# Kernel tuning notes

Measured on AMD Instinct MI355X. Metric: run time of the kernel, lower is better.

The kernel has to match this reference:

```python
import jax, jax.numpy as jnp
import numpy as np
from jax import lax

# 4th-order Butterworth lowpass, scipy.signal.butter(4, 0.2)
B_COEF = np.array([0.004824343357716228, 0.019297373430864913, 0.02894606014629737,
                   0.019297373430864913, 0.004824343357716228], dtype=np.float32)
A_COEF = np.array([1.0, -2.369513007182038, 2.3139884144006453,
                   -1.0546654058785672, 0.18737949236818502], dtype=np.float32)


def setup_inputs() -> dict:
    key = jax.random.key(0)
    x = jax.random.normal(key, (8, 64, 48000), dtype=jnp.float32)
    return {"x": x, "b": jnp.asarray(B_COEF), "a": jnp.asarray(A_COEF)}


def _pad_odd(x, n):
    # Faithful to torch _pad_odd (including its exact slicing on the right side).
    left = 2.0 * x[..., 0:1] - jnp.flip(x[..., 0:n], axis=-1)
    right = 2.0 * x[..., -1:] - jnp.flip(x[..., -(n + 2):-2], axis=-1)
    return jnp.concatenate([left, x, right], axis=-1)


def _lfilter(x, a, b):
    # y[n] = (sum_k b[k] x[n-k] - sum_j a[j] y[n-j]) / a[0]
    a0 = a[0]
    bn = b / a0
    an = a[1:] / a0                      # [N], N = order
    ntaps = b.shape[0]                   # static
    N = a.shape[0] - 1                   # static
    T = x.shape[-1]
    # FIR part: small static tap loop, fully vectorized over batch/time.
    pad = [(0, 0)] * (x.ndim - 1) + [(ntaps - 1, 0)]
    xp = jnp.pad(x, pad)
    f = bn[0] * xp[..., ntaps - 1: ntaps - 1 + T]
    for k in range(1, ntaps):
        f = f + bn[k] * xp[..., ntaps - 1 - k: ntaps - 1 - k + T]
    # IIR recurrence via scan over time.
    f_t = jnp.moveaxis(f, -1, 0)         # [T, B, C]
    init = jnp.zeros(x.shape[:-1] + (N,), x.dtype)  # [B, C, N], y[t-1..t-N]

    def step(carry, ft):
        y = ft - jnp.einsum('k,...k->...', an, carry)
        carry = jnp.concatenate([y[..., None], carry[..., :-1]], axis=-1)
        return carry, y

    _, ys = lax.scan(step, init, f_t)
    return jnp.moveaxis(ys, 0, -1)       # [B, C, T]


def _filtfilt(x, a, b):
    y = _lfilter(x, a, b)
    return jnp.flip(_lfilter(jnp.flip(y, axis=-1), a, b), axis=-1)


def reference(x, b, a):
    scale = jnp.max(jnp.abs(x), axis=-1, keepdims=True)
    xs = x / scale
    padlen = 3 * max(int(a.shape[0]), int(b.shape[0]))  # 15, static
    xp = _pad_odd(xs, padlen)
    y = _filtfilt(xp, a, b)
    y = y[..., padlen:-padlen]
    return y * scale
```

## Files before the change

### kernel.cpp

```cpp
#include <hip/hip_runtime.h>


#define T48   48000
#define LCH   48
#define NCH   1024
#define TP0   48030

__device__ __forceinline__ float padfetch(const float* __restrict__ xs, int p) {
  if (p < 0)        return 0.f;
  if (p < 15)       return 2.f * xs[0] - xs[14 - p];
  if (p < T48 + 15) return xs[p - 15];
  if (p < T48 + 30) return 2.f * xs[T48 - 1] - xs[2 * T48 + 12 - p];
  return 0.f;
}

#define RECUR_STEP(fv, arr, idx)                                                \
  do {                                                                          \
    float u_ = fmaf(na4, r4, (fv));                                             \
    u_ = fmaf(na3, r3, u_); u_ = fmaf(na2, r2, u_); u_ = fmaf(na1, r1, u_);     \
    arr[idx] = u_; r4 = r3; r3 = r2; r2 = r1; r1 = u_;                          \
  } while (0)

__global__ __launch_bounds__(1024, 4) void filtfilt_k(
    const float* __restrict__ x, const float* __restrict__ bco,
    const float* __restrict__ aco, float* __restrict__ out)
{
  __shared__ float Sb[2][NCH][4];
  __shared__ float P[10][16];
  __shared__ float heads[NCH][4];
  __shared__ float stitch[NCH];

  const int c = threadIdx.x;
  const float* __restrict__ xs = x + (size_t)blockIdx.x * T48;
  float* __restrict__ os = out + (size_t)blockIdx.x * T48;

  const float inva0 = 1.f / aco[0];
  const float b0 = bco[0]*inva0, b1 = bco[1]*inva0, b2 = bco[2]*inva0,
              b3 = bco[3]*inva0, b4 = bco[4]*inva0;
  const float na1 = -aco[1]*inva0, na2 = -aco[2]*inva0,
              na3 = -aco[3]*inva0, na4 = -aco[4]*inva0;

  if (c < 4) {
    float r1 = (c==0)?1.f:0.f, r2 = (c==1)?1.f:0.f,
          r3 = (c==2)?1.f:0.f, r4 = (c==3)?1.f:0.f;
#pragma unroll
    for (int n = 0; n < LCH; n++) {
      float h = fmaf(na1, r1, fmaf(na2, r2, fmaf(na3, r3, na4 * r4)));
      r4 = r3; r3 = r2; r2 = r1; r1 = h;
    }
    P[0][0*4+c] = r1; P[0][1*4+c] = r2; P[0][2*4+c] = r3; P[0][3*4+c] = r4;
  }
  __syncthreads();
#pragma unroll
  for (int k = 0; k < 9; k++) {
    float v = 0.f;
    if (c < 16) {
      const int i = c >> 2, j = c & 3;
      v = P[k][i*4+0]*P[k][0*4+j] + P[k][i*4+1]*P[k][1*4+j]
        + P[k][i*4+2]*P[k][2*4+j] + P[k][i*4+3]*P[k][3*4+j];
    }
    if (c < 16) P[k+1][c] = v;
    __syncthreads();
  }

  float y[LCH];
  float r1 = 0.f, r2 = 0.f, r3 = 0.f, r4 = 0.f;
  if (c >= 1 && c <= 999) {
    const float4* __restrict__ xp4 = reinterpret_cast<const float4*>(xs + 48*c - 20);
    float4 pv = xp4[0];
#pragma unroll
    for (int j = 1; j < 14; j++) {
      const float4 t = xp4[j];
      if (4*j-5 >= 0 && 4*j-5 < LCH) {
        float f = fmaf(b0,t.x, fmaf(b1,pv.w, fmaf(b2,pv.z, fmaf(b3,pv.y, b4*pv.x))));
        RECUR_STEP(f, y, 4*j-5);
      }
      if (4*j-4 >= 0 && 4*j-4 < LCH) {
        float f = fmaf(b0,t.y, fmaf(b1,t.x, fmaf(b2,pv.w, fmaf(b3,pv.z, b4*pv.y))));
        RECUR_STEP(f, y, 4*j-4);
      }
      if (4*j-3 >= 0 && 4*j-3 < LCH) {
        float f = fmaf(b0,t.z, fmaf(b1,t.y, fmaf(b2,t.x, fmaf(b3,pv.w, b4*pv.z))));
        RECUR_STEP(f, y, 4*j-3);
      }
      if (4*j-2 >= 0 && 4*j-2 < LCH) {
        float f = fmaf(b0,t.w, fmaf(b1,t.z, fmaf(b2,t.y, fmaf(b3,t.x, b4*pv.w))));
        RECUR_STEP(f, y, 4*j-2);
      }
      pv = t;
    }
  } else if (c == 0 || c == 1000) {
    float w1 = padfetch(xs, 48*c - 1), w2 = padfetch(xs, 48*c - 2),
          w3 = padfetch(xs, 48*c - 3), w4 = padfetch(xs, 48*c - 4);
#pragma unroll
    for (int n = 0; n < LCH; n++) {
      float w0 = padfetch(xs, 48*c + n);
      float f = fmaf(b0,w0, fmaf(b1,w1, fmaf(b2,w2, fmaf(b3,w3, b4*w4))));
      RECUR_STEP(f, y, n);
      w4 = w3; w3 = w2; w2 = w1; w1 = w0;
    }
  } else {
#pragma unroll
    for (int n = 0; n < LCH; n++) y[n] = 0.f;
  }

  {
    Sb[0][c][0] = r1; Sb[0][c][1] = r2; Sb[0][c][2] = r3; Sb[0][c][3] = r4;
    __syncthreads();
#pragma unroll
    for (int k = 0; k < 10; k++) {
      const int off = 1 << k, cu = k & 1, nx = cu ^ 1;
      float t0 = Sb[cu][c][0], t1 = Sb[cu][c][1], t2 = Sb[cu][c][2], t3 = Sb[cu][c][3];
      if (c >= off) {
        float q0 = Sb[cu][c-off][0], q1 = Sb[cu][c-off][1],
              q2 = Sb[cu][c-off][2], q3 = Sb[cu][c-off][3];
        t0 += P[k][0]*q0  + P[k][1]*q1  + P[k][2]*q2  + P[k][3]*q3;
        t1 += P[k][4]*q0  + P[k][5]*q1  + P[k][6]*q2  + P[k][7]*q3;
        t2 += P[k][8]*q0  + P[k][9]*q1  + P[k][10]*q2 + P[k][11]*q3;
        t3 += P[k][12]*q0 + P[k][13]*q1 + P[k][14]*q2 + P[k][15]*q3;
      }
      Sb[nx][c][0] = t0; Sb[nx][c][1] = t1; Sb[nx][c][2] = t2; Sb[nx][c][3] = t3;
      __syncthreads();
    }
  }
  float s0 = 0.f, s1 = 0.f, s2 = 0.f, s3 = 0.f;
  if (c > 0) { s0 = Sb[0][c-1][0]; s1 = Sb[0][c-1][1]; s2 = Sb[0][c-1][2]; s3 = Sb[0][c-1][3]; }

  {
    float h1 = s0, h2 = s1, h3 = s2, h4 = s3;
#pragma unroll
    for (int n = 0; n < LCH; n++) {
      float h = fmaf(na1, h1, fmaf(na2, h2, fmaf(na3, h3, na4 * h4)));
      y[n] += h;
      h4 = h3; h3 = h2; h2 = h1; h1 = h;
    }
  }
  if (c == 1000) {
#pragma unroll
    for (int n = 0; n < LCH; n++) if (48000 + n >= TP0) y[n] = 0.f;
  } else if (c > 1000) {
#pragma unroll
    for (int n = 0; n < LCH; n++) y[n] = 0.f;
  }

  heads[c][0] = y[0]; heads[c][1] = y[1]; heads[c][2] = y[2]; heads[c][3] = y[3];
  __syncthreads();
  float hl[4] = {0.f, 0.f, 0.f, 0.f};
  if (c < NCH - 1) { hl[0] = heads[c+1][0]; hl[1] = heads[c+1][1];
                     hl[2] = heads[c+1][2]; hl[3] = heads[c+1][3]; }

#define YV(i) (((i) < LCH) ? y[(i)] : hl[(i) - LCH])
  float z[LCH];
  r1 = 0.f; r2 = 0.f; r3 = 0.f; r4 = 0.f;
#pragma unroll
  for (int m = 0; m < LCH; m++) {
    float g = fmaf(b0, YV(47-m), fmaf(b1, YV(48-m),
              fmaf(b2, YV(49-m), fmaf(b3, YV(50-m), b4 * YV(51-m)))));
    RECUR_STEP(g, z, m);
  }
#undef YV

  const int d = NCH - 1 - c;
  {
    Sb[0][d][0] = r1; Sb[0][d][1] = r2; Sb[0][d][2] = r3; Sb[0][d][3] = r4;
    __syncthreads();
#pragma unroll
    for (int k = 0; k < 10; k++) {
      const int off = 1 << k, cu = k & 1, nx = cu ^ 1;
      float t0 = Sb[cu][d][0], t1 = Sb[cu][d][1], t2 = Sb[cu][d][2], t3 = Sb[cu][d][3];
      if (d >= off) {
        float q0 = Sb[cu][d-off][0], q1 = Sb[cu][d-off][1],
              q2 = Sb[cu][d-off][2], q3 = Sb[cu][d-off][3];
        t0 += P[k][0]*q0  + P[k][1]*q1  + P[k][2]*q2  + P[k][3]*q3;
        t1 += P[k][4]*q0  + P[k][5]*q1  + P[k][6]*q2  + P[k][7]*q3;
        t2 += P[k][8]*q0  + P[k][9]*q1  + P[k][10]*q2 + P[k][11]*q3;
        t3 += P[k][12]*q0 + P[k][13]*q1 + P[k][14]*q2 + P[k][15]*q3;
      }
      Sb[nx][d][0] = t0; Sb[nx][d][1] = t1; Sb[nx][d][2] = t2; Sb[nx][d][3] = t3;
      __syncthreads();
    }
  }
  float e0 = 0.f, e1 = 0.f, e2 = 0.f, e3 = 0.f;
  if (d > 0) { e0 = Sb[0][d-1][0]; e1 = Sb[0][d-1][1]; e2 = Sb[0][d-1][2]; e3 = Sb[0][d-1][3]; }

  {
    float h1 = e0, h2 = e1, h3 = e2, h4 = e3;
#pragma unroll
    for (int m = 0; m < LCH; m++) {
      float h = fmaf(na1, h1, fmaf(na2, h2, fmaf(na3, h3, na4 * h4)));
      z[m] += h;
      h4 = h3; h3 = h2; h2 = h1; h1 = h;
    }
  }

  stitch[c] = z[0];
  __syncthreads();
  float zp = (c > 0) ? stitch[c-1] : 0.f;
  {
    const int t = 48*c - 16;
    if (t >= 0 && t <= T48 - 4) {
      float4 v = make_float4(zp, z[47], z[46], z[45]);
      *reinterpret_cast<float4*>(os + t) = v;
    }
  }
#pragma unroll
  for (int k = 0; k < 11; k++) {
    const int t = 48*c - 12 + 4*k;
    const int m0 = 44 - 4*k;
    if (t >= 0 && t <= T48 - 4) {
      float4 v = make_float4(z[m0], z[m0-1], z[m0-2], z[m0-3]);
      *reinterpret_cast<float4*>(os + t) = v;
    }
  }
}

extern "C" void kernel_launch(void* const* d_in, const int* in_sizes, int n_in,
                              void* d_out, int out_size, void* d_ws, size_t ws_size,
                              hipStream_t stream) {
  (void)n_in; (void)d_ws; (void)ws_size; (void)out_size;
  const float* x = (const float*)d_in[0];
  const float* b = (const float*)d_in[1];
  const float* a = (const float*)d_in[2];
  float* out = (float*)d_out;
  const int nseq = in_sizes[0] / T48;
  filtfilt_k<<<dim3(nseq), dim3(1024), 0, stream>>>(x, b, a, out);
}
```

Measured before the change: 236.5 us.

## Stage input and output through padded shared memory for coalesced global access

Global loads are restructured so the input is read in four coalesced sections into a padded shared buffer (stride 49 to avoid bank conflicts), and each thread then pulls its 48-sample chunk from LDS instead of doing strided per-thread float4 loads. The output goes the same way: results are scattered into LDS and written back with coalesced per-section stores. The power-matrix setup now uses wave shuffles instead of serialized syncthreads steps, and the scan buffers are packed into float4 and share the staging buffer. The cost is extra syncthreads rounds, LDS traffic and more complex indexing.

```diff
diff --git a/kernel.cpp b/kernel.cpp
--- a/kernel.cpp
+++ b/kernel.cpp
@@ -2,33 +2,19 @@
 
 
 #define T48   48000
+#define TP0   48030
 #define LCH   48
 #define NCH   1024
-#define TP0   48030
-
-__device__ __forceinline__ float padfetch(const float* __restrict__ xs, int p) {
-  if (p < 0)        return 0.f;
-  if (p < 15)       return 2.f * xs[0] - xs[14 - p];
-  if (p < T48 + 15) return xs[p - 15];
-  if (p < T48 + 30) return 2.f * xs[T48 - 1] - xs[2 * T48 + 12 - p];
-  return 0.f;
-}
-
-#define RECUR_STEP(fv, arr, idx)                                                \
-  do {                                                                          \
-    float u_ = fmaf(na4, r4, (fv));                                             \
-    u_ = fmaf(na3, r3, u_); u_ = fmaf(na2, r2, u_); u_ = fmaf(na1, r1, u_);     \
-    arr[idx] = u_; r4 = r3; r3 = r2; r2 = r1; r1 = u_;                          \
-  } while (0)
+#define SECF  12288
+#define OSEC  12000
+#define UF    12560
 
 __global__ __launch_bounds__(1024, 4) void filtfilt_k(
     const float* __restrict__ x, const float* __restrict__ bco,
     const float* __restrict__ aco, float* __restrict__ out)
 {
-  __shared__ float Sb[2][NCH][4];
+  __shared__ __align__(16) float U[UF];
   __shared__ float P[10][16];
-  __shared__ float heads[NCH][4];
-  __shared__ float stitch[NCH];
 
   const int c = threadIdx.x;
   const float* __restrict__ xs = x + (size_t)blockIdx.x * T48;
@@ -40,177 +26,191 @@
   const float na1 = -aco[1]*inva0, na2 = -aco[2]*inva0,
               na3 = -aco[3]*inva0, na4 = -aco[4]*inva0;
 
-  if (c < 4) {
-    float r1 = (c==0)?1.f:0.f, r2 = (c==1)?1.f:0.f,
-          r3 = (c==2)?1.f:0.f, r4 = (c==3)?1.f:0.f;
+  if (c < 64) {
+    const int i = (c >> 2) & 3, j = c & 3;
+    float r1 = (j==0)?1.f:0.f, r2 = (j==1)?1.f:0.f,
+          r3 = (j==2)?1.f:0.f, r4 = (j==3)?1.f:0.f;
 #pragma unroll
     for (int n = 0; n < LCH; n++) {
       float h = fmaf(na1, r1, fmaf(na2, r2, fmaf(na3, r3, na4 * r4)));
       r4 = r3; r3 = r2; r2 = r1; r1 = h;
     }
-    P[0][0*4+c] = r1; P[0][1*4+c] = r2; P[0][2*4+c] = r3; P[0][3*4+c] = r4;
-  }
-  __syncthreads();
-#pragma unroll
-  for (int k = 0; k < 9; k++) {
-    float v = 0.f;
-    if (c < 16) {
-      const int i = c >> 2, j = c & 3;
-      v = P[k][i*4+0]*P[k][0*4+j] + P[k][i*4+1]*P[k][1*4+j]
-        + P[k][i*4+2]*P[k][2*4+j] + P[k][i*4+3]*P[k][3*4+j];
-    }
-    if (c < 16) P[k+1][c] = v;
-    __syncthreads();
-  }
-
-  float y[LCH];
+    float c0 = __shfl(r1, j), c1 = __shfl(r2, j),
+          c2 = __shfl(r3, j), c3 = __shfl(r4, j);
+    float Pv = (i==0)?c0 : (i==1)?c1 : (i==2)?c2 : c3;
+    if (c < 16) P[0][c] = Pv;
+#pragma unroll
+    for (int k = 0; k < 9; k++) {
+      float rA0 = __shfl(Pv, i*4+0), rA1 = __shfl(Pv, i*4+1),
+            rA2 = __shfl(Pv, i*4+2), rA3 = __shfl(Pv, i*4+3);
+      float cB0 = __shfl(Pv, 0*4+j), cB1 = __shfl(Pv, 1*4+j),
+            cB2 = __shfl(Pv, 2*4+j), cB3 = __shfl(Pv, 3*4+j);
+      Pv = rA0*cB0 + rA1*cB1 + rA2*cB2 + rA3*cB3;
+      if (c < 16) P[k+1][c] = Pv;
+    }
+  }
+
+  float A[LCH];
+  float w1 = 0.f, w2 = 0.f, w3 = 0.f, w4 = 0.f;
+  for (int s = 0; s < 4; s++) {
+    __syncthreads();
+    const int p0 = SECF * s;
+#pragma unroll
+    for (int j = 0; j < 13; j++) {
+      int i = 1024*j + c;
+      if (i < SECF + 4) {
+        int p = p0 - 4 + i;
+        int q = p - 15;
+        float v = 0.f;
+        if (q >= 0 && q < T48)               v = xs[q];
+        else if (p >= 0 && p < 15)           v = 2.f*xs[0] - xs[14 - p];
+        else if (p >= T48+15 && p < TP0)     v = 2.f*xs[T48-1] - xs[2*T48 + 12 - p];
+        U[i + i/48] = v;
+      }
+    }
+    __syncthreads();
+    if ((c >> 8) == s) {
+      const int cl = c & 255;
+      const int rb = 49 * cl;
+      w4 = U[rb+0]; w3 = U[rb+1]; w2 = U[rb+2]; w1 = U[rb+3];
+#pragma unroll
+      for (int n = 0; n < LCH; n++) A[n] = U[rb + (n+4) + ((n+4) >> 6 >= 0 ? (n+4)/48 : 0)];
+    }
+  }
+  __syncthreads();
+
   float r1 = 0.f, r2 = 0.f, r3 = 0.f, r4 = 0.f;
-  if (c >= 1 && c <= 999) {
-    const float4* __restrict__ xp4 = reinterpret_cast<const float4*>(xs + 48*c - 20);
-    float4 pv = xp4[0];
-#pragma unroll
-    for (int j = 1; j < 14; j++) {
-      const float4 t = xp4[j];
-      if (4*j-5 >= 0 && 4*j-5 < LCH) {
-        float f = fmaf(b0,t.x, fmaf(b1,pv.w, fmaf(b2,pv.z, fmaf(b3,pv.y, b4*pv.x))));
-        RECUR_STEP(f, y, 4*j-5);
-      }
-      if (4*j-4 >= 0 && 4*j-4 < LCH) {
-        float f = fmaf(b0,t.y, fmaf(b1,t.x, fmaf(b2,pv.w, fmaf(b3,pv.z, b4*pv.y))));
-        RECUR_STEP(f, y, 4*j-4);
-      }
-      if (4*j-3 >= 0 && 4*j-3 < LCH) {
-        float f = fmaf(b0,t.z, fmaf(b1,t.y, fmaf(b2,t.x, fmaf(b3,pv.w, b4*pv.z))));
-        RECUR_STEP(f, y, 4*j-3);
-      }
-      if (4*j-2 >= 0 && 4*j-2 < LCH) {
-        float f = fmaf(b0,t.w, fmaf(b1,t.z, fmaf(b2,t.y, fmaf(b3,t.x, b4*pv.w))));
-        RECUR_STEP(f, y, 4*j-2);
-      }
-      pv = t;
-    }
-  } else if (c == 0 || c == 1000) {
-    float w1 = padfetch(xs, 48*c - 1), w2 = padfetch(xs, 48*c - 2),
-          w3 = padfetch(xs, 48*c - 3), w4 = padfetch(xs, 48*c - 4);
-#pragma unroll
-    for (int n = 0; n < LCH; n++) {
-      float w0 = padfetch(xs, 48*c + n);
-      float f = fmaf(b0,w0, fmaf(b1,w1, fmaf(b2,w2, fmaf(b3,w3, b4*w4))));
-      RECUR_STEP(f, y, n);
-      w4 = w3; w3 = w2; w2 = w1; w1 = w0;
-    }
-  } else {
-#pragma unroll
-    for (int n = 0; n < LCH; n++) y[n] = 0.f;
-  }
+#pragma unroll
+  for (int n = 0; n < LCH; n++) {
+    float xv = A[n];
+    float f = fmaf(b0,xv, fmaf(b1,w1, fmaf(b2,w2, fmaf(b3,w3, b4*w4))));
+    w4 = w3; w3 = w2; w2 = w1; w1 = xv;
+    float u = fmaf(na4, r4, f);
+    u = fmaf(na3, r3, u); u = fmaf(na2, r2, u); u = fmaf(na1, r1, u);
+    A[n] = u; r4 = r3; r3 = r2; r2 = r1; r1 = u;
+  }
+
+  float4* Sb0 = (float4*)U;
+  float4* Sb1 = (float4*)U + 1024;
+  Sb0[c] = make_float4(r1, r2, r3, r4);
+  __syncthreads();
+#pragma unroll
+  for (int k = 0; k < 10; k++) {
+    float4* cur = (k & 1) ? Sb1 : Sb0;
+    float4* nxt = (k & 1) ? Sb0 : Sb1;
+    const int off = 1 << k;
+    float4 t = cur[c];
+    if (c >= off) {
+      float4 q = cur[c - off];
+      t.x += P[k][0]*q.x  + P[k][1]*q.y  + P[k][2]*q.z  + P[k][3]*q.w;
+      t.y += P[k][4]*q.x  + P[k][5]*q.y  + P[k][6]*q.z  + P[k][7]*q.w;
+      t.z += P[k][8]*q.x  + P[k][9]*q.y  + P[k][10]*q.z + P[k][11]*q.w;
+      t.w += P[k][12]*q.x + P[k][13]*q.y + P[k][14]*q.z + P[k][15]*q.w;
+    }
+    nxt[c] = t;
+    __syncthreads();
+  }
+  float4 sv = make_float4(0.f,0.f,0.f,0.f);
+  if (c > 0) sv = Sb0[c-1];
 
   {
-    Sb[0][c][0] = r1; Sb[0][c][1] = r2; Sb[0][c][2] = r3; Sb[0][c][3] = r4;
-    __syncthreads();
-#pragma unroll
-    for (int k = 0; k < 10; k++) {
-      const int off = 1 << k, cu = k & 1, nx = cu ^ 1;
-      float t0 = Sb[cu][c][0], t1 = Sb[cu][c][1], t2 = Sb[cu][c][2], t3 = Sb[cu][c][3];
-      if (c >= off) {
-        float q0 = Sb[cu][c-off][0], q1 = Sb[cu][c-off][1],
-              q2 = Sb[cu][c-off][2], q3 = Sb[cu][c-off][3];
-        t0 += P[k][0]*q0  + P[k][1]*q1  + P[k][2]*q2  + P[k][3]*q3;
-        t1 += P[k][4]*q0  + P[k][5]*q1  + P[k][6]*q2  + P[k][7]*q3;
-        t2 += P[k][8]*q0  + P[k][9]*q1  + P[k][10]*q2 + P[k][11]*q3;
-        t3 += P[k][12]*q0 + P[k][13]*q1 + P[k][14]*q2 + P[k][15]*q3;
-      }
-      Sb[nx][c][0] = t0; Sb[nx][c][1] = t1; Sb[nx][c][2] = t2; Sb[nx][c][3] = t3;
-      __syncthreads();
-    }
-  }
-  float s0 = 0.f, s1 = 0.f, s2 = 0.f, s3 = 0.f;
-  if (c > 0) { s0 = Sb[0][c-1][0]; s1 = Sb[0][c-1][1]; s2 = Sb[0][c-1][2]; s3 = Sb[0][c-1][3]; }
-
-  {
-    float h1 = s0, h2 = s1, h3 = s2, h4 = s3;
+    float h1 = sv.x, h2 = sv.y, h3 = sv.z, h4 = sv.w;
 #pragma unroll
     for (int n = 0; n < LCH; n++) {
       float h = fmaf(na1, h1, fmaf(na2, h2, fmaf(na3, h3, na4 * h4)));
-      y[n] += h;
+      A[n] += h;
       h4 = h3; h3 = h2; h2 = h1; h1 = h;
     }
   }
-  if (c == 1000) {
-#pragma unroll
-    for (int n = 0; n < LCH; n++) if (48000 + n >= TP0) y[n] = 0.f;
-  } else if (c > 1000) {
-#pragma unroll
-    for (int n = 0; n < LCH; n++) y[n] = 0.f;
-  }
-
-  heads[c][0] = y[0]; heads[c][1] = y[1]; heads[c][2] = y[2]; heads[c][3] = y[3];
-  __syncthreads();
-  float hl[4] = {0.f, 0.f, 0.f, 0.f};
-  if (c < NCH - 1) { hl[0] = heads[c+1][0]; hl[1] = heads[c+1][1];
-                     hl[2] = heads[c+1][2]; hl[3] = heads[c+1][3]; }
-
-#define YV(i) (((i) < LCH) ? y[(i)] : hl[(i) - LCH])
-  float z[LCH];
+  if (c >= 1000) {
+#pragma unroll
+    for (int n = 0; n < LCH; n++) if (48*c + n >= TP0) A[n] = 0.f;
+  }
+
+  Sb1[c] = make_float4(A[0], A[1], A[2], A[3]);
+  __syncthreads();
+  float h0 = 0.f, h1v = 0.f, h2v = 0.f, h3v = 0.f;
+  if (c < NCH - 1) { float4 hv = Sb1[c+1]; h0 = hv.x; h1v = hv.y; h2v = hv.z; h3v = hv.w; }
+
+#define YV(i) ((i) < 48 ? A[(i)] : ((i)==48 ? h0 : (i)==49 ? h1v : (i)==50 ? h2v : h3v))
   r1 = 0.f; r2 = 0.f; r3 = 0.f; r4 = 0.f;
 #pragma unroll
   for (int m = 0; m < LCH; m++) {
     float g = fmaf(b0, YV(47-m), fmaf(b1, YV(48-m),
               fmaf(b2, YV(49-m), fmaf(b3, YV(50-m), b4 * YV(51-m)))));
-    RECUR_STEP(g, z, m);
+    float u = fmaf(na4, r4, g);
+    u = fmaf(na3, r3, u); u = fmaf(na2, r2, u); u = fmaf(na1, r1, u);
+    r4 = r3; r3 = r2; r2 = r1; r1 = u;
+    if      (m == 0) h3v = u;
+    else if (m == 1) h2v = u;
+    else if (m == 2) h1v = u;
+    else if (m == 3) h0  = u;
+    else             A[51 - m] = u;
   }
 #undef YV
 
   const int d = NCH - 1 - c;
+  Sb0[d] = make_float4(r1, r2, r3, r4);
+  __syncthreads();
+#pragma unroll
+  for (int k = 0; k < 10; k++) {
+    float4* cur = (k & 1) ? Sb1 : Sb0;
+    float4* nxt = (k & 1) ? Sb0 : Sb1;
+    const int off = 1 << k;
+    float4 t = cur[d];
+    if (d >= off) {
+      float4 q = cur[d - off];
+      t.x += P[k][0]*q.x  + P[k][1]*q.y  + P[k][2]*q.z  + P[k][3]*q.w;
+      t.y += P[k][4]*q.x  + P[k][5]*q.y  + P[k][6]*q.z  + P[k][7]*q.w;
+      t.z += P[k][8]*q.x  + P[k][9]*q.y  + P[k][10]*q.z + P[k][11]*q.w;
+      t.w += P[k][12]*q.x + P[k][13]*q.y + P[k][14]*q.z + P[k][15]*q.w;
+    }
+    nxt[d] = t;
+    __syncthreads();
+  }
+  float4 ev = make_float4(0.f,0.f,0.f,0.f);
+  if (d > 0) ev = Sb0[d-1];
+
   {
-    Sb[0][d][0] = r1; Sb[0][d][1] = r2; Sb[0][d][2] = r3; Sb[0][d][3] = r4;
-    __syncthreads();
-#pragma unroll
-    for (int k = 0; k < 10; k++) {
-      const int off = 1 << k, cu = k & 1, nx = cu ^ 1;
-      float t0 = Sb[cu][d][0], t1 = Sb[cu][d][1], t2 = Sb[cu][d][2], t3 = Sb[cu][d][3];
-      if (d >= off) {
-        float q0 = Sb[cu][d-off][0], q1 = Sb[cu][d-off][1],
-              q2 = Sb[cu][d-off][2], q3 = Sb[cu][d-off][3];
-        t0 += P[k][0]*q0  + P[k][1]*q1  + P[k][2]*q2  + P[k][3]*q3;
-        t1 += P[k][4]*q0  + P[k][5]*q1  + P[k][6]*q2  + P[k][7]*q3;
-        t2 += P[k][8]*q0  + P[k][9]*q1  + P[k][10]*q2 + P[k][11]*q3;
-        t3 += P[k][12]*q0 + P[k][13]*q1 + P[k][14]*q2 + P[k][15]*q3;
+    float g1 = ev.x, g2 = ev.y, g3 = ev.z, g4 = ev.w;
+#pragma unroll
+    for (int m = 0; m < LCH; m++) {
+      float h = fmaf(na1, g1, fmaf(na2, g2, fmaf(na3, g3, na4 * g4)));
+      if      (m == 0) h3v += h;
+      else if (m == 1) h2v += h;
+      else if (m == 2) h1v += h;
+      else if (m == 3) h0  += h;
+      else             A[51 - m] += h;
+      g4 = g3; g3 = g2; g2 = g1; g1 = h;
+    }
+  }
+
+  __syncthreads();
+  const int tb = 48*c - 15;
+  const int sA = (tb < 0 ? 0 : tb / OSEC);
+  const int sB = (tb + 47) / OSEC;
+  for (int s = 0; s < 4; s++) {
+    const int t0 = OSEC * s;
+    if (s == sA || s == sB) {
+      const int RL49 = 49 * (c - 250*s);
+      const int ibase = tb - t0;
+#pragma unroll
+      for (int k = 0; k < 48; k++) {
+        int i = ibase + k;
+        if ((unsigned)i < (unsigned)OSEC) {
+          float v = (k < 44) ? A[k+4]
+                  : (k == 44) ? h0 : (k == 45) ? h1v : (k == 46) ? h2v : h3v;
+          U[RL49 + k - 15 - (k < 15 ? 1 : 0)] = v;
+        }
       }
-      Sb[nx][d][0] = t0; Sb[nx][d][1] = t1; Sb[nx][d][2] = t2; Sb[nx][d][3] = t3;
-      __syncthreads();
-    }
-  }
-  float e0 = 0.f, e1 = 0.f, e2 = 0.f, e3 = 0.f;
-  if (d > 0) { e0 = Sb[0][d-1][0]; e1 = Sb[0][d-1][1]; e2 = Sb[0][d-1][2]; e3 = Sb[0][d-1][3]; }
-
-  {
-    float h1 = e0, h2 = e1, h3 = e2, h4 = e3;
-#pragma unroll
-    for (int m = 0; m < LCH; m++) {
-      float h = fmaf(na1, h1, fmaf(na2, h2, fmaf(na3, h3, na4 * h4)));
-      z[m] += h;
-      h4 = h3; h3 = h2; h2 = h1; h1 = h;
-    }
-  }
-
-  stitch[c] = z[0];
-  __syncthreads();
-  float zp = (c > 0) ? stitch[c-1] : 0.f;
-  {
-    const int t = 48*c - 16;
-    if (t >= 0 && t <= T48 - 4) {
-      float4 v = make_float4(zp, z[47], z[46], z[45]);
-      *reinterpret_cast<float4*>(os + t) = v;
-    }
-  }
-#pragma unroll
-  for (int k = 0; k < 11; k++) {
-    const int t = 48*c - 12 + 4*k;
-    const int m0 = 44 - 4*k;
-    if (t >= 0 && t <= T48 - 4) {
-      float4 v = make_float4(z[m0], z[m0-1], z[m0-2], z[m0-3]);
-      *reinterpret_cast<float4*>(os + t) = v;
-    }
+    }
+    __syncthreads();
+#pragma unroll
+    for (int j = 0; j < 12; j++) {
+      int i = 1024*j + c;
+      if (i < OSEC) os[t0 + i] = U[i + i/48];
+    }
+    __syncthreads();
   }
 }
 
```

Result: faster. 207.1 us (-12.4%).
